# Performance work log

Measured on AMD Instinct MI355X. Metric: run time of the kernel, lower is better.

The kernel has to match this reference:

```python
import math
import jax, jax.numpy as jnp
import numpy as np

B, L, D, H = 256, 32, 512, 512
NEG_INF = -1e9


def setup_inputs() -> dict:
    key = jax.random.key(0)
    ks = jax.random.split(key, 7)
    x = jax.random.normal(ks[0], (B, L, D), dtype=jnp.float32)
    length = jax.random.randint(ks[1], (B,), 2, L + 1)  # valid lengths in [2, L]
    # word_linear: D -> 2H
    W_word = jax.random.normal(ks[2], (2 * H, D), dtype=jnp.float32) * (1.0 / math.sqrt(D))
    b_word = jnp.zeros((2 * H,), dtype=jnp.float32)
    # comp_linear: 2H -> 5H (orthogonal-ish init; scale is fine for a reference)
    W_comp = jax.random.normal(ks[3], (5 * H, 2 * H), dtype=jnp.float32) * (1.0 / math.sqrt(2 * H))
    b_comp = jnp.zeros((5 * H,), dtype=jnp.float32)
    comp_query = jax.random.normal(ks[4], (H,), dtype=jnp.float32) * 0.01
    return {"x": x, "length": length, "W_word": W_word, "b_word": b_word,
            "W_comp": W_comp, "b_comp": b_comp, "comp_query": comp_query}


def _treelstm_compose(hl, cl, hr, cr, W_comp, b_comp):
    # hl/hr: [B, n, H] -> parent h, c: [B, n, H]
    v = jnp.einsum('bnd,kd->bnk', jnp.concatenate([hl, hr], axis=2), W_comp) + b_comp
    i, fl, fr, u, o = jnp.split(v, 5, axis=2)
    c = cl * jax.nn.sigmoid(fl + 1.0) + cr * jax.nn.sigmoid(fr + 1.0) \
        + jnp.tanh(u) * jax.nn.sigmoid(i)
    h = jax.nn.sigmoid(o) * jnp.tanh(c)
    return h, c


def reference(x, length, W_word, b_word, W_comp, b_comp, comp_query):
    length_mask = (jnp.arange(L)[None, :] < length[:, None]).astype(jnp.float32)  # [B, L]
    # leaf states from word_linear (use_leaf_rnn=False path)
    hc = jnp.einsum('bld,kd->blk', x, W_word) + b_word  # [B, L, 2H]
    h, c = jnp.split(hc, 2, axis=2)
    scale = 1.0 / math.sqrt(H)
    for i in range(L - 1):
        new_h, new_c = _treelstm_compose(h[:, :-1], c[:, :-1], h[:, 1:], c[:, 1:], W_comp, b_comp)
        if i < L - 2:
            # eval-mode greedy composition selection (basic.greedy_select)
            logits = jnp.sum(comp_query * new_h, axis=-1) * scale  # [B, L-1-i]
            mask = length_mask[:, i + 1:]
            logits = jnp.where(mask > 0, logits, NEG_INF)
            select = jax.nn.one_hot(jnp.argmax(logits, axis=1), logits.shape[1], dtype=jnp.float32)
            cum = jnp.cumsum(select, axis=1)
            left = (1.0 - cum)[:, :, None]
            right = (cum - select)[:, :, None]
            sel = select[:, :, None]
            new_h = sel * new_h + left * h[:, :-1] + right * h[:, 1:]
            new_c = sel * new_c + left * c[:, :-1] + right * c[:, 1:]
        done = length_mask[:, i + 1][:, None, None]
        h = done * new_h + (1.0 - done) * h[:, :-1]
        c = done * new_c + (1.0 - done) * c[:, :-1]
    return h[:, 0, :]  # final root hidden state [B, H]
```

## Files before the change

kernel.cpp:

```cpp
#include <hip/hip_runtime.h>
#include <cmath>

#define B_   256
#define L_   32
#define H_   512
#define NH5  2560
#define N2   5120
#define SCALE 0.044194173824159216f

__device__ float g_h [B_*L_*H_];
__device__ float g_c [B_*L_*H_];
__device__ float g_al[(size_t)B_*L_*NH5];
__device__ float g_ar[(size_t)B_*L_*NH5];
__device__ float g_logit[B_*L_];
__device__ int   g_list[B_*L_];
__device__ int   g_count[B_];
__device__ int   g_merged[B_];
__device__ int   g_mpos[B_];
__device__ int   g_rows[B_*L_];
__device__ int   g_nrows;
__device__ int   g_mlist[2][B_];
__device__ int   g_cnt[2];

__device__ __forceinline__ float sigm(float x) { return 1.0f / (1.0f + expf(-x)); }

__device__ __forceinline__ void gate4(float* d, const float* __restrict__ a,
                                      const float* __restrict__ b,
                                      const float* __restrict__ bc, int off) {
  float4 x = *(const float4*)(a + off);
  float4 y = *(const float4*)(b + off);
  float4 z = *(const float4*)(bc + off);
  d[0]=x.x+y.x+z.x; d[1]=x.y+y.y+z.y; d[2]=x.z+y.z+z.z; d[3]=x.w+y.w+z.w;
}
__device__ __forceinline__ void gate2(float* d, const float* __restrict__ a,
                                      const float* __restrict__ b,
                                      const float* __restrict__ bc, int off) {
  float2 x = *(const float2*)(a + off);
  float2 y = *(const float2*)(b + off);
  float2 z = *(const float2*)(bc + off);
  d[0]=x.x+y.x+z.x; d[1]=x.y+y.y+z.y;
}

__global__ __launch_bounds__(256) void scan_init(const int* __restrict__ length) {
  __shared__ int sw[4];
  __shared__ int s_off[256];
  __shared__ int s_len[256];
  const int t = threadIdx.x;
  const int len = length[t];
  s_len[t] = len;
  int v = len;
#pragma unroll
  for (int off = 1; off < 64; off <<= 1) {
    int o = __shfl_up(v, off, 64);
    if ((t & 63) >= off) v += o;
  }
  if ((t & 63) == 63) sw[t >> 6] = v;
  __syncthreads();
  int base = 0;
  for (int w = 0; w < (t >> 6); w++) base += sw[w];
  const int incl = base + v;
  s_off[t] = incl - len;
  if (t == 255) g_nrows = incl;
  g_count[t] = len; g_merged[t] = -2; g_mpos[t] = 0;
  if (t == 0) { g_cnt[0] = 0; g_cnt[1] = 0; }
  __syncthreads();
  for (int idx = t; idx < B_*L_; idx += 256) {
    const int b = idx >> 5, s = idx & 31;
    g_list[idx] = s;
    if (s < s_len[b]) g_rows[s_off[b] + s] = idx;
  }
}

template<int MODE>
__global__ __launch_bounds__(256) void gemm_big(
    const float* __restrict__ Aext,
    const float* __restrict__ Bm,
    const float* __restrict__ bias)
{
  const int NR = g_nrows;
  const int bid = blockIdx.x;
  const int xcd = bid & 7, jj = bid >> 3;
  const int ntp = (MODE == 0) ? 1 : 5;
  const int mt = jj / ntp;
  const int nt = xcd * ntp + (jj - mt * ntp);
  const int m0 = mt * 128;
  if (m0 >= NR) return;
  const int n0 = nt * 128;

  const int tid = threadIdx.x;
  const int w = tid >> 6, l = tid & 63;
  const int tx = (w & 1) * 8 + (l & 7);
  const int ty = (w >> 1) * 8 + (l >> 3);

  __shared__ float As[8][128];
  __shared__ float Bs[8][128];

  const int ra = tid >> 1, qa = (tid & 1) * 4;

  const float* Abase = (MODE == 0) ? Aext : g_h;
  int mr = m0 + ra; if (mr >= NR) mr = NR - 1;
  const float* aptr = Abase + (size_t)g_rows[mr] * 512 + qa;

  const float* bptr;
  {
    int nrow = n0 + ra;
    if (MODE == 0) bptr = Bm + (size_t)nrow * 512 + qa;
    else bptr = Bm + (nrow < NH5 ? (size_t)nrow * 1024
                                 : (size_t)(nrow - NH5) * 1024 + 512) + qa;
  }

  float4 av = *(const float4*)(aptr);
  float4 bv = *(const float4*)(bptr);
  float acc[8][8] = {};

  for (int k0 = 0; k0 < 512; k0 += 8) {
    __syncthreads();
    As[qa+0][ra] = av.x; As[qa+1][ra] = av.y; As[qa+2][ra] = av.z; As[qa+3][ra] = av.w;
    Bs[qa+0][ra] = bv.x; Bs[qa+1][ra] = bv.y; Bs[qa+2][ra] = bv.z; Bs[qa+3][ra] = bv.w;
    __syncthreads();
    if (k0 + 8 < 512) {
      av = *(const float4*)(aptr + k0 + 8);
      bv = *(const float4*)(bptr + k0 + 8);
    }
#pragma unroll
    for (int k = 0; k < 8; k++) {
      float af[8], bf[8];
#pragma unroll
      for (int c = 0; c < 2; c++) {
        float4 t = *(const float4*)&As[k][ty*8 + 4*c];
        af[4*c+0]=t.x; af[4*c+1]=t.y; af[4*c+2]=t.z; af[4*c+3]=t.w;
      }
#pragma unroll
      for (int c = 0; c < 2; c++) {
        float4 t = *(const float4*)&Bs[k][tx*8 + 4*c];
        bf[4*c+0]=t.x; bf[4*c+1]=t.y; bf[4*c+2]=t.z; bf[4*c+3]=t.w;
      }
#pragma unroll
      for (int i = 0; i < 8; i++)
#pragma unroll
        for (int j = 0; j < 8; j++)
          acc[i][j] = fmaf(af[i], bf[j], acc[i][j]);
    }
  }

#pragma unroll
  for (int i = 0; i < 8; i++) {
    int mrow = m0 + ty*8 + i;
    if (mrow >= NR) continue;
    int crow = g_rows[mrow];
#pragma unroll
    for (int j = 0; j < 8; j++) {
      int n = n0 + tx*8 + j;
      float v = acc[i][j];
      if (MODE == 0) {
        v += bias[n];
        if (n < H_) g_h[(size_t)crow*H_ + n]        = v;
        else        g_c[(size_t)crow*H_ + (n - H_)] = v;
      } else {
        if (n < NH5) g_al[(size_t)crow*NH5 + n]         = v;
        else         g_ar[(size_t)crow*NH5 + (n - NH5)] = v;
      }
    }
  }
}

__global__ __launch_bounds__(256) void iter0_logits(const int* __restrict__ length,
                                                    const float* __restrict__ bc,
                                                    const float* __restrict__ qv) {
  __shared__ float sred[4];
  const int p = blockIdx.x, b = blockIdx.y;
  if (p >= length[b] - 1) return;
  const float* al = g_al + (size_t)(b*L_ + p)*NH5;
  const float* ar = g_ar + (size_t)(b*L_ + p + 1)*NH5;
  const float* cl = g_c  + (size_t)(b*L_ + p)*H_;
  const float* cr = g_c  + (size_t)(b*L_ + p + 1)*H_;
  const int j0 = threadIdx.x * 2;
  float vi[2], vfl[2], vfr[2], vu[2], vo[2];
  gate2(vi , al, ar, bc,        j0);
  gate2(vfl, al, ar, bc, H_   + j0);
  gate2(vfr, al, ar, bc, 2*H_ + j0);
  gate2(vu , al, ar, bc, 3*H_ + j0);
  gate2(vo , al, ar, bc, 4*H_ + j0);
  float2 CL = *(const float2*)(cl + j0);
  float2 CR = *(const float2*)(cr + j0);
  float2 Q  = *(const float2*)(qv + j0);
  const float clv[2] = {CL.x, CL.y};
  const float crv[2] = {CR.x, CR.y};
  const float qq [2] = {Q.x, Q.y};
  float part = 0.f;
#pragma unroll
  for (int u = 0; u < 2; ++u) {
    float c = clv[u]*sigm(vfl[u]+1.f) + crv[u]*sigm(vfr[u]+1.f) + tanhf(vu[u])*sigm(vi[u]);
    float h = sigm(vo[u])*tanhf(c);
    part = fmaf(qq[u], h, part);
  }
#pragma unroll
  for (int off = 32; off; off >>= 1) part += __shfl_down(part, off, 64);
  if ((threadIdx.x & 63) == 0) sred[threadIdx.x >> 6] = part;
  __syncthreads();
  if (threadIdx.x == 0)
    g_logit[b*L_ + p] = (sred[0]+sred[1]+sred[2]+sred[3]) * SCALE;
}

__global__ __launch_bounds__(512) void select_merge(int iter,
    const int* __restrict__ length,
    const float* __restrict__ bc,
    const float* __restrict__ qv,
    float* __restrict__ out)
{
  __shared__ float sred[4];
  __shared__ int s_sel[3];
  const int b = blockIdx.x, tid = threadIdx.x;
  const bool fin = (iter == L_-2);
  if (b == 0 && tid == 0) g_cnt[(iter & 1) ^ 1] = 0;

  const int m     = g_count[b];
  const int pslot = g_merged[b];
  const int ppos  = g_mpos[b];
  int* list = g_list + b*L_;

  if (iter > 0 && pslot >= 0) {
    const int half = tid >> 7, lt = tid & 127;
    int sl = -1, sr = -1;
    if (half == 0)      { if (ppos > 0)     { sl = list[ppos-1]; sr = list[ppos];   } }
    else if (half == 1) { if (ppos < m - 1) { sl = list[ppos];   sr = list[ppos+1]; } }
    float part = 0.f;
    if (sl >= 0) {
      const float* al = g_al + (size_t)(b*L_+sl)*NH5;
      const float* ar = g_ar + (size_t)(b*L_+sr)*NH5;
      const float* cl = g_c  + (size_t)(b*L_+sl)*H_;
      const float* cr = g_c  + (size_t)(b*L_+sr)*H_;
      const int j0 = lt * 4;
      float vi[4], vfl[4], vfr[4], vu[4], vo[4];
      gate4(vi , al, ar, bc,        j0);
      gate4(vfl, al, ar, bc, H_   + j0);
      gate4(vfr, al, ar, bc, 2*H_ + j0);
      gate4(vu , al, ar, bc, 3*H_ + j0);
      gate4(vo , al, ar, bc, 4*H_ + j0);
      float4 CL = *(const float4*)(cl + j0);
      float4 CR = *(const float4*)(cr + j0);
      float4 Q  = *(const float4*)(qv + j0);
      const float clv[4] = {CL.x,CL.y,CL.z,CL.w};
      const float crv[4] = {CR.x,CR.y,CR.z,CR.w};
      const float qq [4] = {Q.x,Q.y,Q.z,Q.w};
#pragma unroll
      for (int u = 0; u < 4; ++u) {
        float c = clv[u]*sigm(vfl[u]+1.f) + crv[u]*sigm(vfr[u]+1.f) + tanhf(vu[u])*sigm(vi[u]);
        float h = sigm(vo[u])*tanhf(c);
        part = fmaf(qq[u], h, part);
      }
    }
#pragma unroll
    for (int off = 32; off; off >>= 1) part += __shfl_down(part, off, 64);
    if ((tid & 63) == 0 && tid < 256) sred[tid >> 6] = part;
    __syncthreads();
    if (tid == 0   && ppos > 0)     g_logit[b*L_ + list[ppos-1]] = (sred[0]+sred[1])*SCALE;
    if (tid == 128 && ppos < m - 1) g_logit[b*L_ + list[ppos]]   = (sred[2]+sred[3])*SCALE;
  }

  const bool active = iter < (length[b] - 1);
  if (!active) {
    if (tid == 0) g_merged[b] = -1;
    if (fin)
      out[(size_t)b*H_ + tid] = g_h[(size_t)(b*L_)*H_ + tid];
    return;
  }

  __syncthreads();

  if (tid < 64) {
    float lg = -1e30f; int idx = tid;
    if (tid < m - 1) lg = g_logit[b*L_ + list[tid]];
#pragma unroll
    for (int off = 32; off; off >>= 1) {
      float olg = __shfl_down(lg, off, 64);
      int   oid = __shfl_down(idx, off, 64);
      if (olg > lg || (olg == lg && oid < idx)) { lg = olg; idx = oid; }
    }
    if (tid == 0) { s_sel[0] = idx; s_sel[1] = list[idx]; s_sel[2] = list[idx+1]; }
  }
  __syncthreads();
  const int pos = s_sel[0], sl = s_sel[1], sr = s_sel[2];

  {
    const float* al = g_al + (size_t)(b*L_+sl)*NH5;
    const float* ar = g_ar + (size_t)(b*L_+sr)*NH5;
    float*       cl = g_c  + (size_t)(b*L_+sl)*H_;
    const float* cr = g_c  + (size_t)(b*L_+sr)*H_;
    float*       hl = g_h  + (size_t)(b*L_+sl)*H_;
    const int j = tid;
    float vi  = al[j]       + ar[j]       + bc[j];
    float vfl = al[H_+j]    + ar[H_+j]    + bc[H_+j];
    float vfr = al[2*H_+j]  + ar[2*H_+j]  + bc[2*H_+j];
    float vu  = al[3*H_+j]  + ar[3*H_+j]  + bc[3*H_+j];
    float vo  = al[4*H_+j]  + ar[4*H_+j]  + bc[4*H_+j];
    float c = cl[j]*sigm(vfl+1.f) + cr[j]*sigm(vfr+1.f) + tanhf(vu)*sigm(vi);
    float h = sigm(vo)*tanhf(c);
    cl[j] = c; hl[j] = h;
    if (fin)
      out[(size_t)b*H_ + j] = h;
  }
  if (tid == 0) {
    for (int n = pos+1; n < m-1; n++) list[n] = list[n+1];
    g_count[b]  = m - 1;
    g_merged[b] = sl;
    g_mpos[b]   = pos;
    int k = atomicAdd(&g_cnt[iter & 1], 1);
    g_mlist[iter & 1][k] = b;
  }
}

__global__ __launch_bounds__(256) void gemm_iter(int par, const float* __restrict__ Wc)
{
  const int nact = g_cnt[par];
  const int bid = blockIdx.x;
  const int xcd = bid & 7, jj = bid >> 3;
  const int mt = jj / 10;
  const int nt = xcd * 10 + (jj - mt * 10);
  const int m0 = mt * 32;
  if (m0 >= nact) return;
  const int n0 = nt * 64;
  const int tid = threadIdx.x;

  __shared__ float As[2][32][32];
  __shared__ float Bs[2][32][64];

  const int ra = tid >> 3, qa = (tid & 7) * 4;
  int mr = m0 + ra; if (mr >= nact) mr = nact - 1;
  const int bbA = g_mlist[par][mr];
  const float* aptr = g_h + (size_t)(bbA*L_ + g_merged[bbA]) * 512 + qa;

  const int rb = tid >> 2, qb = (tid & 3) * 8;
  const int nr = n0 + rb;
  const float* bptr = (nr < NH5) ? Wc + (size_t)nr * 1024 + qb
                                 : Wc + (size_t)(nr - NH5) * 1024 + 512 + qb;

  const int tx = tid & 15, ty = tid >> 4;

  float4 av  = *(const float4*)(aptr);
  float4 bv0 = *(const float4*)(bptr);
  float4 bv1 = *(const float4*)(bptr + 4);
  As[0][qa+0][ra]=av.x;  As[0][qa+1][ra]=av.y;  As[0][qa+2][ra]=av.z;  As[0][qa+3][ra]=av.w;
  Bs[0][qb+0][rb]=bv0.x; Bs[0][qb+1][rb]=bv0.y; Bs[0][qb+2][rb]=bv0.z; Bs[0][qb+3][rb]=bv0.w;
  Bs[0][qb+4][rb]=bv1.x; Bs[0][qb+5][rb]=bv1.y; Bs[0][qb+6][rb]=bv1.z; Bs[0][qb+7][rb]=bv1.w;
  __syncthreads();

  float acc[2][4] = {};
  for (int s = 0; s < 16; ++s) {
    const int cur = s & 1;
    if (s < 15) {
      const int ko = 32 * (s + 1);
      av  = *(const float4*)(aptr + ko);
      bv0 = *(const float4*)(bptr + ko);
      bv1 = *(const float4*)(bptr + ko + 4);
    }
#pragma unroll
    for (int k = 0; k < 32; k++) {
      float2 a2 = *(const float2*)&As[cur][k][ty*2];
      float4 b4 = *(const float4*)&Bs[cur][k][tx*4];
      acc[0][0] = fmaf(a2.x, b4.x, acc[0][0]);
      acc[0][1] = fmaf(a2.x, b4.y, acc[0][1]);
      acc[0][2] = fmaf(a2.x, b4.z, acc[0][2]);
      acc[0][3] = fmaf(a2.x, b4.w, acc[0][3]);
      acc[1][0] = fmaf(a2.y, b4.x, acc[1][0]);
      acc[1][1] = fmaf(a2.y, b4.y, acc[1][1]);
      acc[1][2] = fmaf(a2.y, b4.z, acc[1][2]);
      acc[1][3] = fmaf(a2.y, b4.w, acc[1][3]);
    }
    if (s < 15) {
      const int nx = cur ^ 1;
      As[nx][qa+0][ra]=av.x;  As[nx][qa+1][ra]=av.y;  As[nx][qa+2][ra]=av.z;  As[nx][qa+3][ra]=av.w;
      Bs[nx][qb+0][rb]=bv0.x; Bs[nx][qb+1][rb]=bv0.y; Bs[nx][qb+2][rb]=bv0.z; Bs[nx][qb+3][rb]=bv0.w;
      Bs[nx][qb+4][rb]=bv1.x; Bs[nx][qb+5][rb]=bv1.y; Bs[nx][qb+6][rb]=bv1.z; Bs[nx][qb+7][rb]=bv1.w;
      __syncthreads();
    }
  }

#pragma unroll
  for (int i = 0; i < 2; i++) {
    int mrow = m0 + ty*2 + i;
    if (mrow >= nact) continue;
    int bb = g_mlist[par][mrow];
    size_t base = (size_t)(bb*L_ + g_merged[bb]) * NH5;
    int n = n0 + tx*4;
    float4 v = make_float4(acc[i][0], acc[i][1], acc[i][2], acc[i][3]);
    if (n < NH5) *(float4*)(g_al + base + n)         = v;
    else         *(float4*)(g_ar + base + (n - NH5)) = v;
  }
}

extern "C" void kernel_launch(void* const* d_in, const int* in_sizes, int n_in,
                              void* d_out, int out_size, void* d_ws, size_t ws_size,
                              hipStream_t stream)
{
  (void)in_sizes; (void)n_in; (void)out_size; (void)d_ws; (void)ws_size;
  const float* x      = (const float*)d_in[0];
  const int*   length = (const int*)  d_in[1];
  const float* W_word = (const float*)d_in[2];
  const float* b_word = (const float*)d_in[3];
  const float* W_comp = (const float*)d_in[4];
  const float* b_comp = (const float*)d_in[5];
  const float* q      = (const float*)d_in[6];
  float* out = (float*)d_out;

  scan_init<<<1, 256, 0, stream>>>(length);

  gemm_big<0><<<8*64,  256, 0, stream>>>(x, W_word, b_word);
  gemm_big<1><<<40*64, 256, 0, stream>>>(nullptr, W_comp, nullptr);

  iter0_logits<<<dim3(L_-1, B_), 256, 0, stream>>>(length, b_comp, q);

  for (int i = 0; i < L_-1; i++) {
    select_merge<<<B_, 512, 0, stream>>>(i, length, b_comp, q, out);
    if (i < L_-2)
      gemm_iter<<<640, 256, 0, stream>>>(i & 1, W_comp);
  }
}
```

Baseline: 1.570 ms.

## Restructure GEMM kernels to single-wavefront blocks with larger per-thread tiles

Both GEMM kernels are rewritten to launch 64-thread blocks, one wavefront each. gemm_big now uses a 64x128 tile with an 8x16 per-thread accumulator, and gemm_iter uses a 32x64 tile with a 4x8 per-thread accumulator and stores vectorised as float4. The aim is more FMA work per shared-memory load and fewer cross-wave barriers. In exchange it raises register pressure, drops the double buffering in gemm_iter, and reduces threads per block, which may lower latency hiding.

```diff
diff --git a/kernel.cpp b/kernel.cpp
--- a/kernel.cpp
+++ b/kernel.cpp
@@ -72,7 +72,7 @@
 }
 
 template<int MODE>
-__global__ __launch_bounds__(256) void gemm_big(
+__global__ __launch_bounds__(64) void gemm_big(
     const float* __restrict__ Aext,
     const float* __restrict__ Bm,
     const float* __restrict__ bias)
@@ -83,82 +83,87 @@
   const int ntp = (MODE == 0) ? 1 : 5;
   const int mt = jj / ntp;
   const int nt = xcd * ntp + (jj - mt * ntp);
-  const int m0 = mt * 128;
+  const int m0 = mt * 64;
   if (m0 >= NR) return;
   const int n0 = nt * 128;
 
   const int tid = threadIdx.x;
-  const int w = tid >> 6, l = tid & 63;
-  const int tx = (w & 1) * 8 + (l & 7);
-  const int ty = (w >> 1) * 8 + (l >> 3);
-
-  __shared__ float As[8][128];
+  const int tx = tid & 7;
+  const int ty = tid >> 3;
+
+  __shared__ float As[8][64];
   __shared__ float Bs[8][128];
 
-  const int ra = tid >> 1, qa = (tid & 1) * 4;
-
+  int mr = m0 + tid; if (mr >= NR) mr = NR - 1;
   const float* Abase = (MODE == 0) ? Aext : g_h;
-  int mr = m0 + ra; if (mr >= NR) mr = NR - 1;
-  const float* aptr = Abase + (size_t)g_rows[mr] * 512 + qa;
-
-  const float* bptr;
+  const float* aptr = Abase + (size_t)g_rows[mr] * 512;
+
+  const float* bp0; const float* bp1;
   {
-    int nrow = n0 + ra;
-    if (MODE == 0) bptr = Bm + (size_t)nrow * 512 + qa;
-    else bptr = Bm + (nrow < NH5 ? (size_t)nrow * 1024
-                                 : (size_t)(nrow - NH5) * 1024 + 512) + qa;
-  }
-
-  float4 av = *(const float4*)(aptr);
-  float4 bv = *(const float4*)(bptr);
-  float acc[8][8] = {};
+    int r0 = n0 + tid, r1 = n0 + tid + 64;
+    if (MODE == 0) { bp0 = Bm + (size_t)r0 * 512; bp1 = Bm + (size_t)r1 * 512; }
+    else {
+      bp0 = Bm + (r0 < NH5 ? (size_t)r0 * 1024 : (size_t)(r0 - NH5) * 1024 + 512);
+      bp1 = Bm + (r1 < NH5 ? (size_t)r1 * 1024 : (size_t)(r1 - NH5) * 1024 + 512);
+    }
+  }
+
+  float4 a0 = *(const float4*)(aptr),     a1 = *(const float4*)(aptr + 4);
+  float4 b00 = *(const float4*)(bp0),     b01 = *(const float4*)(bp0 + 4);
+  float4 b10 = *(const float4*)(bp1),     b11 = *(const float4*)(bp1 + 4);
+  float acc[8][16] = {};
 
   for (int k0 = 0; k0 < 512; k0 += 8) {
     __syncthreads();
-    As[qa+0][ra] = av.x; As[qa+1][ra] = av.y; As[qa+2][ra] = av.z; As[qa+3][ra] = av.w;
-    Bs[qa+0][ra] = bv.x; Bs[qa+1][ra] = bv.y; Bs[qa+2][ra] = bv.z; Bs[qa+3][ra] = bv.w;
+    As[0][tid]=a0.x;  As[1][tid]=a0.y;  As[2][tid]=a0.z;  As[3][tid]=a0.w;
+    As[4][tid]=a1.x;  As[5][tid]=a1.y;  As[6][tid]=a1.z;  As[7][tid]=a1.w;
+    Bs[0][tid]=b00.x; Bs[1][tid]=b00.y; Bs[2][tid]=b00.z; Bs[3][tid]=b00.w;
+    Bs[4][tid]=b01.x; Bs[5][tid]=b01.y; Bs[6][tid]=b01.z; Bs[7][tid]=b01.w;
+    Bs[0][tid+64]=b10.x; Bs[1][tid+64]=b10.y; Bs[2][tid+64]=b10.z; Bs[3][tid+64]=b10.w;
+    Bs[4][tid+64]=b11.x; Bs[5][tid+64]=b11.y; Bs[6][tid+64]=b11.z; Bs[7][tid+64]=b11.w;
     __syncthreads();
     if (k0 + 8 < 512) {
-      av = *(const float4*)(aptr + k0 + 8);
-      bv = *(const float4*)(bptr + k0 + 8);
+      a0  = *(const float4*)(aptr + k0 + 8);  a1  = *(const float4*)(aptr + k0 + 12);
+      b00 = *(const float4*)(bp0 + k0 + 8);   b01 = *(const float4*)(bp0 + k0 + 12);
+      b10 = *(const float4*)(bp1 + k0 + 8);   b11 = *(const float4*)(bp1 + k0 + 12);
     }
 #pragma unroll
     for (int k = 0; k < 8; k++) {
-      float af[8], bf[8];
-#pragma unroll
-      for (int c = 0; c < 2; c++) {
-        float4 t = *(const float4*)&As[k][ty*8 + 4*c];
-        af[4*c+0]=t.x; af[4*c+1]=t.y; af[4*c+2]=t.z; af[4*c+3]=t.w;
+      float4 A0 = *(const float4*)&As[k][ty*4];
+      float4 A1 = *(const float4*)&As[k][ty*4 + 32];
+      float af[8] = {A0.x,A0.y,A0.z,A0.w, A1.x,A1.y,A1.z,A1.w};
+      float bf[16];
+#pragma unroll
+      for (int q = 0; q < 4; q++) {
+        float4 Bq = *(const float4*)&Bs[k][tx*4 + 32*q];
+        bf[q*4+0]=Bq.x; bf[q*4+1]=Bq.y; bf[q*4+2]=Bq.z; bf[q*4+3]=Bq.w;
       }
 #pragma unroll
-      for (int c = 0; c < 2; c++) {
-        float4 t = *(const float4*)&Bs[k][tx*8 + 4*c];
-        bf[4*c+0]=t.x; bf[4*c+1]=t.y; bf[4*c+2]=t.z; bf[4*c+3]=t.w;
-      }
-#pragma unroll
-      for (int i = 0; i < 8; i++)
-#pragma unroll
-        for (int j = 0; j < 8; j++)
-          acc[i][j] = fmaf(af[i], bf[j], acc[i][j]);
-    }
-  }
-
-#pragma unroll
-  for (int i = 0; i < 8; i++) {
-    int mrow = m0 + ty*8 + i;
+      for (int r = 0; r < 8; r++)
+#pragma unroll
+        for (int c = 0; c < 16; c++)
+          acc[r][c] = fmaf(af[r], bf[c], acc[r][c]);
+    }
+  }
+
+#pragma unroll
+  for (int r = 0; r < 8; r++) {
+    int mrow = m0 + 32*(r>>2) + ty*4 + (r&3);
     if (mrow >= NR) continue;
     int crow = g_rows[mrow];
 #pragma unroll
-    for (int j = 0; j < 8; j++) {
-      int n = n0 + tx*8 + j;
-      float v = acc[i][j];
+    for (int q = 0; q < 4; q++) {
+      int n = n0 + 32*q + tx*4;
+      float4 v = make_float4(acc[r][q*4+0], acc[r][q*4+1],
+                             acc[r][q*4+2], acc[r][q*4+3]);
       if (MODE == 0) {
-        v += bias[n];
-        if (n < H_) g_h[(size_t)crow*H_ + n]        = v;
-        else        g_c[(size_t)crow*H_ + (n - H_)] = v;
+        float4 b4 = *(const float4*)(bias + n);
+        v.x += b4.x; v.y += b4.y; v.z += b4.z; v.w += b4.w;
+        if (n < H_) *(float4*)(g_h + (size_t)crow*H_ + n)        = v;
+        else        *(float4*)(g_c + (size_t)crow*H_ + (n - H_)) = v;
       } else {
-        if (n < NH5) g_al[(size_t)crow*NH5 + n]         = v;
-        else         g_ar[(size_t)crow*NH5 + (n - NH5)] = v;
+        if (n < NH5) *(float4*)(g_al + (size_t)crow*NH5 + n)         = v;
+        else         *(float4*)(g_ar + (size_t)crow*NH5 + (n - NH5)) = v;
       }
     }
   }
@@ -310,7 +315,7 @@
   }
 }
 
-__global__ __launch_bounds__(256) void gemm_iter(int par, const float* __restrict__ Wc)
+__global__ __launch_bounds__(64) void gemm_iter(int par, const float* __restrict__ Wc)
 {
   const int nact = g_cnt[par];
   const int bid = blockIdx.x;
@@ -321,71 +326,76 @@
   if (m0 >= nact) return;
   const int n0 = nt * 64;
   const int tid = threadIdx.x;
-
-  __shared__ float As[2][32][32];
-  __shared__ float Bs[2][32][64];
-
-  const int ra = tid >> 3, qa = (tid & 7) * 4;
-  int mr = m0 + ra; if (mr >= nact) mr = nact - 1;
+  const int tx = tid & 7;
+  const int ty = tid >> 3;
+
+  __shared__ float As[32][32];
+  __shared__ float Bs[32][64];
+
+  const int ar = tid & 31, ah = (tid >> 5) * 16;
+  int mr = m0 + ar; if (mr >= nact) mr = nact - 1;
   const int bbA = g_mlist[par][mr];
-  const float* aptr = g_h + (size_t)(bbA*L_ + g_merged[bbA]) * 512 + qa;
-
-  const int rb = tid >> 2, qb = (tid & 3) * 8;
-  const int nr = n0 + rb;
-  const float* bptr = (nr < NH5) ? Wc + (size_t)nr * 1024 + qb
-                                 : Wc + (size_t)(nr - NH5) * 1024 + 512 + qb;
-
-  const int tx = tid & 15, ty = tid >> 4;
-
-  float4 av  = *(const float4*)(aptr);
-  float4 bv0 = *(const float4*)(bptr);
-  float4 bv1 = *(const float4*)(bptr + 4);
-  As[0][qa+0][ra]=av.x;  As[0][qa+1][ra]=av.y;  As[0][qa+2][ra]=av.z;  As[0][qa+3][ra]=av.w;
-  Bs[0][qb+0][rb]=bv0.x; Bs[0][qb+1][rb]=bv0.y; Bs[0][qb+2][rb]=bv0.z; Bs[0][qb+3][rb]=bv0.w;
-  Bs[0][qb+4][rb]=bv1.x; Bs[0][qb+5][rb]=bv1.y; Bs[0][qb+6][rb]=bv1.z; Bs[0][qb+7][rb]=bv1.w;
-  __syncthreads();
-
-  float acc[2][4] = {};
-  for (int s = 0; s < 16; ++s) {
-    const int cur = s & 1;
-    if (s < 15) {
-      const int ko = 32 * (s + 1);
-      av  = *(const float4*)(aptr + ko);
-      bv0 = *(const float4*)(bptr + ko);
-      bv1 = *(const float4*)(bptr + ko + 4);
+  const float* aptr = g_h + (size_t)(bbA*L_ + g_merged[bbA]) * 512 + ah;
+
+  const int nr = n0 + tid;
+  const float* bptr = (nr < NH5) ? Wc + (size_t)nr * 1024
+                                 : Wc + (size_t)(nr - NH5) * 1024 + 512;
+
+  float4 av[4], bv[8];
+#pragma unroll
+  for (int u = 0; u < 4; u++) av[u] = *(const float4*)(aptr + 4*u);
+#pragma unroll
+  for (int u = 0; u < 8; u++) bv[u] = *(const float4*)(bptr + 4*u);
+
+  float acc[4][8] = {};
+  for (int k0 = 0; k0 < 512; k0 += 32) {
+    __syncthreads();
+#pragma unroll
+    for (int u = 0; u < 4; u++) {
+      As[ah+4*u+0][ar]=av[u].x; As[ah+4*u+1][ar]=av[u].y;
+      As[ah+4*u+2][ar]=av[u].z; As[ah+4*u+3][ar]=av[u].w;
+    }
+#pragma unroll
+    for (int u = 0; u < 8; u++) {
+      Bs[4*u+0][tid]=bv[u].x; Bs[4*u+1][tid]=bv[u].y;
+      Bs[4*u+2][tid]=bv[u].z; Bs[4*u+3][tid]=bv[u].w;
+    }
+    __syncthreads();
+    if (k0 + 32 < 512) {
+#pragma unroll
+      for (int u = 0; u < 4; u++) av[u] = *(const float4*)(aptr + k0 + 32 + 4*u);
+#pragma unroll
+      for (int u = 0; u < 8; u++) bv[u] = *(const float4*)(bptr + k0 + 32 + 4*u);
     }
 #pragma unroll
     for (int k = 0; k < 32; k++) {
-      float2 a2 = *(const float2*)&As[cur][k][ty*2];
-      float4 b4 = *(const float4*)&Bs[cur][k][tx*4];
-      acc[0][0] = fmaf(a2.x, b4.x, acc[0][0]);
-      acc[0][1] = fmaf(a2.x, b4.y, acc[0][1]);
-      acc[0][2] = fmaf(a2.x, b4.z, acc[0][2]);
-      acc[0][3] = fmaf(a2.x, b4.w, acc[0][3]);
-      acc[1][0] = fmaf(a2.y, b4.x, acc[1][0]);
-      acc[1][1] = fmaf(a2.y, b4.y, acc[1][1]);
-      acc[1][2] = fmaf(a2.y, b4.z, acc[1][2]);
-      acc[1][3] = fmaf(a2.y, b4.w, acc[1][3]);
-    }
-    if (s < 15) {
-      const int nx = cur ^ 1;
-      As[nx][qa+0][ra]=av.x;  As[nx][qa+1][ra]=av.y;  As[nx][qa+2][ra]=av.z;  As[nx][qa+3][ra]=av.w;
-      Bs[nx][qb+0][rb]=bv0.x; Bs[nx][qb+1][rb]=bv0.y; Bs[nx][qb+2][rb]=bv0.z; Bs[nx][qb+3][rb]=bv0.w;
-      Bs[nx][qb+4][rb]=bv1.x; Bs[nx][qb+5][rb]=bv1.y; Bs[nx][qb+6][rb]=bv1.z; Bs[nx][qb+7][rb]=bv1.w;
-      __syncthreads();
-    }
-  }
-
-#pragma unroll
-  for (int i = 0; i < 2; i++) {
-    int mrow = m0 + ty*2 + i;
+      float4 A0 = *(const float4*)&As[k][ty*4];
+      float4 B0 = *(const float4*)&Bs[k][tx*4];
+      float4 B1 = *(const float4*)&Bs[k][tx*4 + 32];
+      float af[4] = {A0.x,A0.y,A0.z,A0.w};
+      float bf[8] = {B0.x,B0.y,B0.z,B0.w, B1.x,B1.y,B1.z,B1.w};
+#pragma unroll
+      for (int i = 0; i < 4; i++)
+#pragma unroll
+        for (int c = 0; c < 8; c++)
+          acc[i][c] = fmaf(af[i], bf[c], acc[i][c]);
+    }
+  }
+
+#pragma unroll
+  for (int i = 0; i < 4; i++) {
+    int mrow = m0 + ty*4 + i;
     if (mrow >= nact) continue;
     int bb = g_mlist[par][mrow];
     size_t base = (size_t)(bb*L_ + g_merged[bb]) * NH5;
-    int n = n0 + tx*4;
-    float4 v = make_float4(acc[i][0], acc[i][1], acc[i][2], acc[i][3]);
-    if (n < NH5) *(float4*)(g_al + base + n)         = v;
-    else         *(float4*)(g_ar + base + (n - NH5)) = v;
+#pragma unroll
+    for (int q = 0; q < 2; q++) {
+      int n = n0 + 32*q + tx*4;
+      float4 v = make_float4(acc[i][q*4+0], acc[i][q*4+1],
+                             acc[i][q*4+2], acc[i][q*4+3]);
+      if (n < NH5) *(float4*)(g_al + base + n)         = v;
+      else         *(float4*)(g_ar + base + (n - NH5)) = v;
+    }
   }
 }
 
@@ -405,14 +415,14 @@
 
   scan_init<<<1, 256, 0, stream>>>(length);
 
-  gemm_big<0><<<8*64,  256, 0, stream>>>(x, W_word, b_word);
-  gemm_big<1><<<40*64, 256, 0, stream>>>(nullptr, W_comp, nullptr);
+  gemm_big<0><<<8*128,  64, 0, stream>>>(x, W_word, b_word);
+  gemm_big<1><<<40*128, 64, 0, stream>>>(nullptr, W_comp, nullptr);
 
   iter0_logits<<<dim3(L_-1, B_), 256, 0, stream>>>(length, b_comp, q);
 
   for (int i = 0; i < L_-1; i++) {
     select_merge<<<B_, 512, 0, stream>>>(i, length, b_comp, q, out);
     if (i < L_-2)
-      gemm_iter<<<640, 256, 0, stream>>>(i & 1, W_comp);
-  }
-}
+      gemm_iter<<<640, 64, 0, stream>>>(i & 1, W_comp);
+  }
+}
```

Result: slower. 1.795 ms (+14.4%).
